# Performance work log

Hardware: AMD Instinct MI355X
Metric: run time of the kernel (lower is better)

Reference implementation:

```python
import jax, jax.numpy as jnp
import numpy as np

EPS = 1e-5
BANDLIMIT = 0.5
STEP_SCALE = 1.0


def _ln(x, g, b):
    mu = jnp.mean(x, axis=-1, keepdims=True)
    var = jnp.mean(jnp.square(x - mu), axis=-1, keepdims=True)
    return (x - mu) * jax.lax.rsqrt(var + EPS) * g + b


def _s5(u, Lambda_re, Lambda_im, B_re, B_im, C_re, C_im, D, log_step):
    # u: [N, T, C]; diagonal S5 SSM with ZOH discretization and parallel scan.
    Lam = Lambda_re + 1j * Lambda_im                      # [P] complex
    Bm = B_re + 1j * B_im                                  # [P, C]
    Cm = C_re + 1j * C_im                                  # [C, P]
    step = STEP_SCALE * jnp.exp(log_step)                  # [P]
    Lam_bar = jnp.exp(Lam * step)                          # [P]
    B_bar = ((Lam_bar - 1.0) / Lam)[:, None] * Bm          # [P, C]
    # bandlimit mask on output projection (freqs use un-scaled step)
    freqs = jnp.exp(log_step) * jnp.abs(Lambda_im) / (2.0 * jnp.pi)
    Cm = Cm * jnp.where(freqs < BANDLIMIT * 0.5, 1.0, 0.0)[None, :]
    Bu = jnp.einsum('ntc,pc->ntp', u.astype(B_bar.dtype), B_bar)  # [N,T,P] complex
    A = jnp.broadcast_to(Lam_bar, Bu.shape)

    def op(e1, e2):
        a1, b1 = e1
        a2, b2 = e2
        return a2 * a1, a2 * b1 + b2

    _, xs = jax.lax.associative_scan(op, (A, Bu), axis=1)   # x_t = Lam_bar*x_{t-1} + B_bar u_t (x_0 = 0)
    y = jnp.einsum('ntp,cp->ntc', xs, Cm).real + u * D
    return y


def setup_inputs() -> dict:
    key = jax.random.key(0)
    ks = jax.random.split(key, 16)
    B, T, H, W = 2, 15, 192, 192
    C, P = 16, 16
    sC = 1.0 / np.sqrt(C)
    sP = 1.0 / np.sqrt(P)
    inp = {}
    inp['x'] = jax.random.normal(ks[0], (B, T, H, W), dtype=jnp.float32)
    # input_proj: Linear(1, C)
    inp['w_in'] = jax.random.normal(ks[1], (C,), dtype=jnp.float32)
    inp['b_in'] = jnp.zeros((C,), dtype=jnp.float32)
    # S5Block attn_norm
    inp['attn_gamma'] = jnp.ones((C,), dtype=jnp.float32)
    inp['attn_beta'] = jnp.zeros((C,), dtype=jnp.float32)
    # S5 SSM parameters (stable: Re(Lambda) < 0)
    inp['Lambda_re'] = -jax.random.uniform(ks[2], (P,), jnp.float32, 0.1, 1.0)
    inp['Lambda_im'] = jnp.pi * jnp.arange(P, dtype=jnp.float32)
    inp['B_re'] = sC * jax.random.normal(ks[3], (P, C), dtype=jnp.float32)
    inp['B_im'] = sC * jax.random.normal(ks[4], (P, C), dtype=jnp.float32)
    inp['C_re'] = sP * jax.random.normal(ks[5], (C, P), dtype=jnp.float32)
    inp['C_im'] = sP * jax.random.normal(ks[6], (C, P), dtype=jnp.float32)
    inp['D'] = jax.random.normal(ks[7], (C,), dtype=jnp.float32)
    inp['log_step'] = jax.random.uniform(ks[8], (P,), jnp.float32, np.log(1e-3), np.log(0.1))
    # S5Block FFN (GEGLU, ff_mult=1.0, no bias)
    inp['ff_gamma'] = jnp.ones((C,), dtype=jnp.float32)
    inp['ff_beta'] = jnp.zeros((C,), dtype=jnp.float32)
    inp['W_enc'] = sC * jax.random.normal(ks[9], (2 * C, C), dtype=jnp.float32)
    inp['W_dec'] = sC * jax.random.normal(ks[10], (C, C), dtype=jnp.float32)
    # output_proj: LayerNorm(C) + Linear(C, C)
    inp['out_gamma'] = jnp.ones((C,), dtype=jnp.float32)
    inp['out_beta'] = jnp.zeros((C,), dtype=jnp.float32)
    inp['W_out'] = sC * jax.random.normal(ks[11], (C, C), dtype=jnp.float32)
    inp['b_out'] = jnp.zeros((C,), dtype=jnp.float32)
    return inp


def reference(x, w_in, b_in, attn_gamma, attn_beta, Lambda_re, Lambda_im,
              B_re, B_im, C_re, C_im, D, log_step,
              ff_gamma, ff_beta, W_enc, W_dec,
              out_gamma, out_beta, W_out, b_out):
    b, t, h, w = x.shape
    C = w_in.shape[0]
    # (b t h w) -> (b h w) t 1 -> Linear(1, C)
    u = jnp.transpose(x, (0, 2, 3, 1)).reshape(b * h * w, t)          # [N, T]
    u = u[:, :, None] * w_in + b_in                                     # [N, T, C]
    # --- S5Block ---
    fx = _ln(u, attn_gamma, attn_beta)
    s5_out = _s5(fx, Lambda_re, Lambda_im, B_re, B_im, C_re, C_im, D, log_step)
    z = jax.nn.gelu(s5_out, approximate=False) + fx
    fx2 = _ln(z, ff_gamma, ff_beta)
    enc = fx2 @ W_enc.T                                                 # [N, T, 2C]
    a, g = enc[..., :C], enc[..., C:]
    z2 = (a * jax.nn.gelu(g, approximate=False)) @ W_dec.T + fx2
    # aggregation = 'last'
    agg = z2[:, -1, :]                                                  # [N, C]
    # output_proj
    out = _ln(agg, out_gamma, out_beta) @ W_out.T + b_out               # [N, C]
    y = jnp.transpose(out.reshape(b, h, w, C), (0, 3, 1, 2))            # [B, C, H, W]
    return y
```

## Files before the change

### kernel.cpp

```cpp
#include <hip/hip_runtime.h>
#include <math.h>

#define HW_TOT 36864
#define T_LEN  15
#define NSEQ   73728


__device__ __forceinline__ float gelu_exact(float x){
  float ax = fabsf(x) * 0.7071067811865476f;
  float t  = 1.0f / (1.0f + 0.3275911f * ax);
  float poly = t*(0.254829592f + t*(-0.284496736f + t*(1.421413741f +
               t*(-1.453152027f + t*1.061405429f))));
  float er = 1.0f - poly * __expf(-ax*ax);
  er = copysignf(er, x);
  return 0.5f * x * (1.0f + er);
}

__global__ void __launch_bounds__(64) ssm_setup(
    const float* __restrict__ w_in, const float* __restrict__ b_in,
    const float* __restrict__ ag,   const float* __restrict__ ab,
    const float* __restrict__ Lre,  const float* __restrict__ Lim,
    const float* __restrict__ Bre,  const float* __restrict__ Bim,
    const float* __restrict__ Cre,  const float* __restrict__ Cim,
    const float* __restrict__ Dv,   const float* __restrict__ ls,
    const float* __restrict__ ffg,  const float* __restrict__ ffb,
    const float* __restrict__ Wenc, const float* __restrict__ Wdec,
    const float* __restrict__ og,   const float* __restrict__ ob,
    const float* __restrict__ Wout, const float* __restrict__ bout,
    float* __restrict__ ws)
{
  const int tid = threadIdx.x;

  float mw = 0.f, mb = 0.f;
  for (int c = 0; c < 16; ++c){ mw += w_in[c]; mb += b_in[c]; }
  mw *= 0.0625f; mb *= 0.0625f;
  float Saa = 0.f, Sad = 0.f, Sdd = 0.f;
  for (int c = 0; c < 16; ++c){
    float a = w_in[c]-mw, d = b_in[c]-mb;
    Saa += a*a; Sad += a*d; Sdd += d*d;
  }
  Saa *= 0.0625f; Sad *= 0.0625f; Sdd *= 0.0625f;
  if (tid == 0){ ws[128]=Saa; ws[129]=2.f*Sad; ws[130]=Sdd; ws[131]=0.f; }

  if (tid < 16){
    int c = tid;
    float a = w_in[c]-mw, d = b_in[c]-mb, g = ag[c];
    ws[132+c] = a*g;
    ws[148+c] = d*g;
    ws[164+c] = ab[c];
    ws[180+c] = Dv[c];
  }

  if (tid < 16){
    int p = tid;
    float step = expf(ls[p]);
    float lr = Lre[p], li = Lim[p];
    float er = expf(lr*step);
    float th = li*step;
    float Lbr = er*cosf(th), Lbi = er*sinf(th);
    ws[96+p] = Lbr; ws[112+p] = Lbi;
    float inv = 1.f/(lr*lr + li*li);
    float gr = Lbr - 1.f, gi = Lbi;
    float fr = (gr*lr + gi*li)*inv;
    float fi = (gi*lr - gr*li)*inv;
    float P1r=0,P1i=0,P2r=0,P2i=0,P3r=0,P3i=0;
    for (int c = 0; c < 16; ++c){
      float br = Bre[p*16+c], bi = Bim[p*16+c];
      float Bbr = fr*br - fi*bi, Bbi = fr*bi + fi*br;
      float a = w_in[c]-mw, d = b_in[c]-mb, g = ag[c];
      float f1 = a*g, f2 = d*g, f3 = ab[c];
      P1r += f1*Bbr; P1i += f1*Bbi;
      P2r += f2*Bbr; P2i += f2*Bbi;
      P3r += f3*Bbr; P3i += f3*Bbi;
    }
    ws[ 0+p]=P1r; ws[16+p]=P1i; ws[32+p]=P2r;
    ws[48+p]=P2i; ws[64+p]=P3r; ws[80+p]=P3i;
  }

  for (int k = tid; k < 256; k += 64){
    int p = k & 15;
    float step = expf(ls[p]);
    float freq = step * fabsf(Lim[p]) * 0.15915494309189535f;
    float m = (freq < 0.25f) ? 1.f : 0.f;
    ws[196+k] = Cre[k]*m;
    ws[452+k] = Cim[k]*m;
  }
  for (int k = tid; k < 512; k += 64) ws[ 708+k] = Wenc[k];
  for (int k = tid; k < 256; k += 64) ws[1220+k] = Wdec[k];
  for (int k = tid; k < 256; k += 64) ws[1540+k] = Wout[k];
  if (tid < 16){
    ws[1476+tid] = ffg[tid];
    ws[1492+tid] = ffb[tid];
    ws[1508+tid] = og[tid];
    ws[1524+tid] = ob[tid];
    ws[1796+tid] = bout[tid];
  }
}

__global__ void __launch_bounds__(64) ssm_main(
    const float* __restrict__ x, const float* __restrict__ ws,
    float* __restrict__ out)
{
  const int n   = blockIdx.x * 64 + threadIdx.x;
  const int b   = (n >= HW_TOT) ? 1 : 0;
  const int rem = n - b * HW_TOT;

  const float* xp = x + (size_t)b * (T_LEN * HW_TOT) + rem;
  float xv[T_LEN];
#pragma unroll
  for (int t = 0; t < T_LEN; ++t) xv[t] = xp[(size_t)t * HW_TOT];

  const float Saa = ws[128], Sad2 = ws[129], Sdd = ws[130];
  float P1r[16],P1i[16],P2r[16],P2i[16],P3r[16],P3i[16],Lr[16],Li[16];
#pragma unroll
  for (int p = 0; p < 16; ++p){
    P1r[p]=ws[p];    P1i[p]=ws[16+p];
    P2r[p]=ws[32+p]; P2i[p]=ws[48+p];
    P3r[p]=ws[64+p]; P3i[p]=ws[80+p];
    Lr[p] =ws[96+p]; Li[p] =ws[112+p];
  }

  float sre[16], sim_[16];
#pragma unroll
  for (int p = 0; p < 16; ++p){ sre[p]=0.f; sim_[p]=0.f; }

  float rstdL = 0.f, s1L = 0.f;
#pragma unroll
  for (int t = 0; t < T_LEN; ++t){
    const float xvt  = xv[t];
    const float var  = fmaf(xvt, fmaf(xvt, Saa, Sad2), Sdd);
    const float rstd = rsqrtf(var + 1e-5f);
    const float s1   = rstd * xvt;
#pragma unroll
    for (int p = 0; p < 16; ++p){
      const float br = fmaf(s1, P1r[p], fmaf(rstd, P2r[p], P3r[p]));
      const float bi = fmaf(s1, P1i[p], fmaf(rstd, P2i[p], P3i[p]));
      const float nr = fmaf(Lr[p], sre[p], fmaf(-Li[p], sim_[p], br));
      const float ni = fmaf(Lr[p], sim_[p], fmaf( Li[p], sre[p], bi));
      sre[p] = nr; sim_[p] = ni;
    }
    rstdL = rstd; s1L = s1;
  }

  float fx[16];
#pragma unroll
  for (int c = 0; c < 16; ++c)
    fx[c] = fmaf(s1L, ws[132+c], fmaf(rstdL, ws[148+c], ws[164+c]));

  float z[16];
#pragma unroll
  for (int c = 0; c < 16; ++c){
    float acc = fx[c] * ws[180+c];
#pragma unroll
    for (int p = 0; p < 16; ++p){
      acc = fmaf(sre[p],   ws[196 + c*16 + p], acc);
      acc = fmaf(-sim_[p], ws[452 + c*16 + p], acc);
    }
    z[c] = gelu_exact(acc) + fx[c];
  }

  float mu = 0.f;
#pragma unroll
  for (int c = 0; c < 16; ++c) mu += z[c];
  mu *= 0.0625f;
  float vr = 0.f;
#pragma unroll
  for (int c = 0; c < 16; ++c){ float d = z[c]-mu; vr = fmaf(d,d,vr); }
  vr *= 0.0625f;
  float rs = rsqrtf(vr + 1e-5f);
  float fx2[16];
#pragma unroll
  for (int c = 0; c < 16; ++c)
    fx2[c] = fmaf((z[c]-mu)*rs, ws[1476+c], ws[1492+c]);

  float hg[16];
#pragma unroll
  for (int c = 0; c < 16; ++c){
    float a = 0.f, g = 0.f;
#pragma unroll
    for (int k = 0; k < 16; ++k){
      a = fmaf(fx2[k], ws[708 + c*16 + k], a);
      g = fmaf(fx2[k], ws[708 + (16+c)*16 + k], g);
    }
    hg[c] = a * gelu_exact(g);
  }

  float z2[16];
#pragma unroll
  for (int c = 0; c < 16; ++c){
    float acc = fx2[c];
#pragma unroll
    for (int k = 0; k < 16; ++k) acc = fmaf(hg[k], ws[1220 + c*16 + k], acc);
    z2[c] = acc;
  }

  float mu3 = 0.f;
#pragma unroll
  for (int c = 0; c < 16; ++c) mu3 += z2[c];
  mu3 *= 0.0625f;
  float v3 = 0.f;
#pragma unroll
  for (int c = 0; c < 16; ++c){ float d = z2[c]-mu3; v3 = fmaf(d,d,v3); }
  v3 *= 0.0625f;
  float rs3 = rsqrtf(v3 + 1e-5f);
  float q[16];
#pragma unroll
  for (int c = 0; c < 16; ++c)
    q[c] = fmaf((z2[c]-mu3)*rs3, ws[1508+c], ws[1524+c]);

  float* op = out + (size_t)b * (16*HW_TOT) + rem;
#pragma unroll
  for (int c = 0; c < 16; ++c){
    float acc = ws[1796+c];
#pragma unroll
    for (int k = 0; k < 16; ++k) acc = fmaf(q[k], ws[1540 + c*16 + k], acc);
    op[(size_t)c * HW_TOT] = acc;
  }
}

extern "C" void kernel_launch(void* const* d_in, const int* in_sizes, int n_in,
                              void* d_out, int out_size, void* d_ws, size_t ws_size,
                              hipStream_t stream)
{
  const float* x    = (const float*)d_in[0];
  const float* w_in = (const float*)d_in[1];
  const float* b_in = (const float*)d_in[2];
  const float* ag   = (const float*)d_in[3];
  const float* ab   = (const float*)d_in[4];
  const float* Lre  = (const float*)d_in[5];
  const float* Lim  = (const float*)d_in[6];
  const float* Bre  = (const float*)d_in[7];
  const float* Bim  = (const float*)d_in[8];
  const float* Cre  = (const float*)d_in[9];
  const float* Cim  = (const float*)d_in[10];
  const float* Dv   = (const float*)d_in[11];
  const float* ls   = (const float*)d_in[12];
  const float* ffg  = (const float*)d_in[13];
  const float* ffb  = (const float*)d_in[14];
  const float* Wenc = (const float*)d_in[15];
  const float* Wdec = (const float*)d_in[16];
  const float* og   = (const float*)d_in[17];
  const float* ob   = (const float*)d_in[18];
  const float* Wout = (const float*)d_in[19];
  const float* bout = (const float*)d_in[20];
  float* ws  = (float*)d_ws;
  float* out = (float*)d_out;

  ssm_setup<<<1, 64, 0, stream>>>(w_in, b_in, ag, ab, Lre, Lim, Bre, Bim,
                                  Cre, Cim, Dv, ls, ffg, ffb, Wenc, Wdec,
                                  og, ob, Wout, bout, ws);
  ssm_main<<<NSEQ/64, 64, 0, stream>>>(x, ws, out);
}
```

Before: 135.1 us.

## Factor SSM scan into two input-driven recurrences and stage params in LDS

The per-step SSM input is split algebraically into a term scaled by s1, a term scaled by rstd, and a constant term. The constant term's scan contribution is precomputed in the setup kernel as a geometric sum. The main kernel then runs two scalar-driven complex recurrences and projects them through P1/P2 only once at the end, which drops the per-step complex B projections. All workspace parameters are also staged into shared memory per block instead of being read from global memory. This adds a block-wide copy and a barrier, and holds four complex accumulator arrays in registers.

```diff
diff --git a/kernel.cpp b/kernel.cpp
--- a/kernel.cpp
+++ b/kernel.cpp
@@ -4,6 +4,7 @@
 #define HW_TOT 36864
 #define T_LEN  15
 #define NSEQ   73728
+#define WS_N   1812
 
 
 __device__ __forceinline__ float gelu_exact(float x){
@@ -58,7 +59,7 @@
     float er = expf(lr*step);
     float th = li*step;
     float Lbr = er*cosf(th), Lbi = er*sinf(th);
-    ws[96+p] = Lbr; ws[112+p] = Lbi;
+    ws[0+p] = Lbr; ws[16+p] = Lbi;
     float inv = 1.f/(lr*lr + li*li);
     float gr = Lbr - 1.f, gi = Lbi;
     float fr = (gr*lr + gi*li)*inv;
@@ -73,8 +74,17 @@
       P2r += f2*Bbr; P2i += f2*Bbi;
       P3r += f3*Bbr; P3i += f3*Bbi;
     }
-    ws[ 0+p]=P1r; ws[16+p]=P1i; ws[32+p]=P2r;
-    ws[48+p]=P2i; ws[64+p]=P3r; ws[80+p]=P3i;
+    ws[32+p]=P1r; ws[48+p]=P1i;
+    ws[64+p]=P2r; ws[80+p]=P2i;
+    float kr=1.f, ki=0.f, cr_=1.f, ci_=0.f;
+    for (int j = 1; j < T_LEN; ++j){
+      float nr = cr_*Lbr - ci_*Lbi;
+      float ni = cr_*Lbi + ci_*Lbr;
+      cr_ = nr; ci_ = ni;
+      kr += cr_; ki += ci_;
+    }
+    ws[ 96+p] = P3r*kr - P3i*ki;
+    ws[112+p] = P3r*ki + P3i*kr;
   }
 
   for (int k = tid; k < 256; k += 64){
@@ -87,12 +97,12 @@
   }
   for (int k = tid; k < 512; k += 64) ws[ 708+k] = Wenc[k];
   for (int k = tid; k < 256; k += 64) ws[1220+k] = Wdec[k];
-  for (int k = tid; k < 256; k += 64) ws[1540+k] = Wout[k];
+  for (int k = tid; k < 256; k += 64) ws[1476+k] = Wout[k];
   if (tid < 16){
-    ws[1476+tid] = ffg[tid];
-    ws[1492+tid] = ffb[tid];
-    ws[1508+tid] = og[tid];
-    ws[1524+tid] = ob[tid];
+    ws[1732+tid] = ffg[tid];
+    ws[1748+tid] = ffb[tid];
+    ws[1764+tid] = og[tid];
+    ws[1780+tid] = ob[tid];
     ws[1796+tid] = bout[tid];
   }
 }
@@ -101,6 +111,9 @@
     const float* __restrict__ x, const float* __restrict__ ws,
     float* __restrict__ out)
 {
+  __shared__ float sm[WS_N];
+  for (int k = threadIdx.x; k < WS_N; k += 64) sm[k] = ws[k];
+
   const int n   = blockIdx.x * 64 + threadIdx.x;
   const int b   = (n >= HW_TOT) ? 1 : 0;
   const int rem = n - b * HW_TOT;
@@ -110,19 +123,16 @@
 #pragma unroll
   for (int t = 0; t < T_LEN; ++t) xv[t] = xp[(size_t)t * HW_TOT];
 
-  const float Saa = ws[128], Sad2 = ws[129], Sdd = ws[130];
-  float P1r[16],P1i[16],P2r[16],P2i[16],P3r[16],P3i[16],Lr[16],Li[16];
-#pragma unroll
-  for (int p = 0; p < 16; ++p){
-    P1r[p]=ws[p];    P1i[p]=ws[16+p];
-    P2r[p]=ws[32+p]; P2i[p]=ws[48+p];
-    P3r[p]=ws[64+p]; P3i[p]=ws[80+p];
-    Lr[p] =ws[96+p]; Li[p] =ws[112+p];
-  }
-
-  float sre[16], sim_[16];
-#pragma unroll
-  for (int p = 0; p < 16; ++p){ sre[p]=0.f; sim_[p]=0.f; }
+  __syncthreads();
+
+  float Lr[16], Li[16];
+#pragma unroll
+  for (int p = 0; p < 16; ++p){ Lr[p] = sm[p]; Li[p] = sm[16+p]; }
+  const float Saa = sm[128], Sad2 = sm[129], Sdd = sm[130];
+
+  float A1r[16], A1i[16], A2r[16], A2i[16];
+#pragma unroll
+  for (int p = 0; p < 16; ++p){ A1r[p]=0.f; A1i[p]=0.f; A2r[p]=0.f; A2i[p]=0.f; }
 
   float rstdL = 0.f, s1L = 0.f;
 #pragma unroll
@@ -133,28 +143,42 @@
     const float s1   = rstd * xvt;
 #pragma unroll
     for (int p = 0; p < 16; ++p){
-      const float br = fmaf(s1, P1r[p], fmaf(rstd, P2r[p], P3r[p]));
-      const float bi = fmaf(s1, P1i[p], fmaf(rstd, P2i[p], P3i[p]));
-      const float nr = fmaf(Lr[p], sre[p], fmaf(-Li[p], sim_[p], br));
-      const float ni = fmaf(Lr[p], sim_[p], fmaf( Li[p], sre[p], bi));
-      sre[p] = nr; sim_[p] = ni;
+      float n1r = fmaf(Lr[p], A1r[p], fmaf(-Li[p], A1i[p], s1));
+      float n1i = fmaf(Lr[p], A1i[p], Li[p]*A1r[p]);
+      A1r[p] = n1r; A1i[p] = n1i;
+      float n2r = fmaf(Lr[p], A2r[p], fmaf(-Li[p], A2i[p], rstd));
+      float n2i = fmaf(Lr[p], A2i[p], Li[p]*A2r[p]);
+      A2r[p] = n2r; A2i[p] = n2i;
     }
     rstdL = rstd; s1L = s1;
   }
 
+  float sre[16], sim_[16];
+#pragma unroll
+  for (int p = 0; p < 16; ++p){
+    float p1r = sm[32+p], p1i = sm[48+p];
+    float p2r = sm[64+p], p2i = sm[80+p];
+    float r = sm[96+p], im = sm[112+p];
+    r  = fmaf(p1r, A1r[p], fmaf(-p1i, A1i[p], r));
+    r  = fmaf(p2r, A2r[p], fmaf(-p2i, A2i[p], r));
+    im = fmaf(p1r, A1i[p], fmaf( p1i, A1r[p], im));
+    im = fmaf(p2r, A2i[p], fmaf( p2i, A2r[p], im));
+    sre[p] = r; sim_[p] = im;
+  }
+
   float fx[16];
 #pragma unroll
   for (int c = 0; c < 16; ++c)
-    fx[c] = fmaf(s1L, ws[132+c], fmaf(rstdL, ws[148+c], ws[164+c]));
+    fx[c] = fmaf(s1L, sm[132+c], fmaf(rstdL, sm[148+c], sm[164+c]));
 
   float z[16];
 #pragma unroll
   for (int c = 0; c < 16; ++c){
-    float acc = fx[c] * ws[180+c];
+    float acc = fx[c] * sm[180+c];
 #pragma unroll
     for (int p = 0; p < 16; ++p){
-      acc = fmaf(sre[p],   ws[196 + c*16 + p], acc);
-      acc = fmaf(-sim_[p], ws[452 + c*16 + p], acc);
+      acc = fmaf(sre[p],   sm[196 + c*16 + p], acc);
+      acc = fmaf(-sim_[p], sm[452 + c*16 + p], acc);
     }
     z[c] = gelu_exact(acc) + fx[c];
   }
@@ -171,7 +195,7 @@
   float fx2[16];
 #pragma unroll
   for (int c = 0; c < 16; ++c)
-    fx2[c] = fmaf((z[c]-mu)*rs, ws[1476+c], ws[1492+c]);
+    fx2[c] = fmaf((z[c]-mu)*rs, sm[1732+c], sm[1748+c]);
 
   float hg[16];
 #pragma unroll
@@ -179,8 +203,8 @@
     float a = 0.f, g = 0.f;
 #pragma unroll
     for (int k = 0; k < 16; ++k){
-      a = fmaf(fx2[k], ws[708 + c*16 + k], a);
-      g = fmaf(fx2[k], ws[708 + (16+c)*16 + k], g);
+      a = fmaf(fx2[k], sm[708 + c*16 + k], a);
+      g = fmaf(fx2[k], sm[708 + (16+c)*16 + k], g);
     }
     hg[c] = a * gelu_exact(g);
   }
@@ -190,7 +214,7 @@
   for (int c = 0; c < 16; ++c){
     float acc = fx2[c];
 #pragma unroll
-    for (int k = 0; k < 16; ++k) acc = fmaf(hg[k], ws[1220 + c*16 + k], acc);
+    for (int k = 0; k < 16; ++k) acc = fmaf(hg[k], sm[1220 + c*16 + k], acc);
     z2[c] = acc;
   }
 
@@ -203,17 +227,17 @@
   for (int c = 0; c < 16; ++c){ float d = z2[c]-mu3; v3 = fmaf(d,d,v3); }
   v3 *= 0.0625f;
   float rs3 = rsqrtf(v3 + 1e-5f);
-  float q[16];
+  float qv[16];
 #pragma unroll
   for (int c = 0; c < 16; ++c)
-    q[c] = fmaf((z2[c]-mu3)*rs3, ws[1508+c], ws[1524+c]);
+    qv[c] = fmaf((z2[c]-mu3)*rs3, sm[1764+c], sm[1780+c]);
 
   float* op = out + (size_t)b * (16*HW_TOT) + rem;
 #pragma unroll
   for (int c = 0; c < 16; ++c){
-    float acc = ws[1796+c];
-#pragma unroll
-    for (int k = 0; k < 16; ++k) acc = fmaf(q[k], ws[1540 + c*16 + k], acc);
+    float acc = sm[1796+c];
+#pragma unroll
+    for (int k = 0; k < 16; ++k) acc = fmaf(qv[k], sm[1476 + c*16 + k], acc);
     op[(size_t)c * HW_TOT] = acc;
   }
 }
```

New measurement: 122.4 us. 1.1x faster.

## Collapse SSM scan into precomputed per-timestep kernels and process two sequences per thread

Applied to the files above, without the earlier changes.

The setup kernel now precomputes, for each output channel and timestep, the combined effect of the input projection, Lambda powers and the masked C projection. The main kernel then computes the last-step SSM output as a linear combination of per-timestep terms, which replaces the 16-state complex recurrence and the C projection. The main kernel also stages the weight table in shared memory and handles two sequences per thread so each weight read is reused. This cuts per-thread arithmetic, but the grid shrinks to 576 blocks of 64 threads and register pressure rises.

```diff
diff --git a/kernel.cpp b/kernel.cpp
--- a/kernel.cpp
+++ b/kernel.cpp
@@ -4,7 +4,23 @@
 #define HW_TOT 36864
 #define T_LEN  15
 #define NSEQ   73728
-
+#define NBLK   576
+
+#define OFF_F1    4
+#define OFF_F2    20
+#define OFF_F3    36
+#define OFF_D     52
+#define OFF_G3    68
+#define OFF_G12   84
+#define OFF_WENC  596
+#define OFF_WDEC  1108
+#define OFF_WOUT  1364
+#define OFF_FFG   1620
+#define OFF_FFB   1636
+#define OFF_OG    1652
+#define OFF_OB    1668
+#define OFF_BOUT  1684
+#define SM_N      1700
 
 __device__ __forceinline__ float gelu_exact(float x){
   float ax = fabsf(x) * 0.7071067811865476f;
@@ -29,6 +45,8 @@
     const float* __restrict__ Wout, const float* __restrict__ bout,
     float* __restrict__ ws)
 {
+  __shared__ float U1r[240], U1i[240], U2r[240], U2i[240];
+  __shared__ float Cr[256], Ci[256], Qr[16], Qi[16];
   const int tid = threadIdx.x;
 
   float mw = 0.f, mb = 0.f;
@@ -40,15 +58,20 @@
     Saa += a*a; Sad += a*d; Sdd += d*d;
   }
   Saa *= 0.0625f; Sad *= 0.0625f; Sdd *= 0.0625f;
-  if (tid == 0){ ws[128]=Saa; ws[129]=2.f*Sad; ws[130]=Sdd; ws[131]=0.f; }
+  if (tid == 0){ ws[0]=Saa; ws[1]=2.f*Sad; ws[2]=Sdd; ws[3]=0.f; }
 
   if (tid < 16){
     int c = tid;
     float a = w_in[c]-mw, d = b_in[c]-mb, g = ag[c];
-    ws[132+c] = a*g;
-    ws[148+c] = d*g;
-    ws[164+c] = ab[c];
-    ws[180+c] = Dv[c];
+    ws[OFF_F1+c] = a*g;
+    ws[OFF_F2+c] = d*g;
+    ws[OFF_F3+c] = ab[c];
+    ws[OFF_D +c] = Dv[c];
+    ws[OFF_FFG+c] = ffg[c];
+    ws[OFF_FFB+c] = ffb[c];
+    ws[OFF_OG +c] = og[c];
+    ws[OFF_OB +c] = ob[c];
+    ws[OFF_BOUT+c] = bout[c];
   }
 
   if (tid < 16){
@@ -58,7 +81,6 @@
     float er = expf(lr*step);
     float th = li*step;
     float Lbr = er*cosf(th), Lbi = er*sinf(th);
-    ws[96+p] = Lbr; ws[112+p] = Lbi;
     float inv = 1.f/(lr*lr + li*li);
     float gr = Lbr - 1.f, gi = Lbi;
     float fr = (gr*lr + gi*li)*inv;
@@ -73,8 +95,23 @@
       P2r += f2*Bbr; P2i += f2*Bbi;
       P3r += f3*Bbr; P3i += f3*Bbi;
     }
-    ws[ 0+p]=P1r; ws[16+p]=P1i; ws[32+p]=P2r;
-    ws[48+p]=P2i; ws[64+p]=P3r; ws[80+p]=P3i;
+    float c1r=P1r, c1i=P1i, c2r=P2r, c2i=P2i;
+    U1r[p*15+0]=c1r; U1i[p*15+0]=c1i;
+    U2r[p*15+0]=c2r; U2i[p*15+0]=c2i;
+    float kr=1.f, ki=0.f, pr=1.f, pi=0.f;
+    for (int j = 1; j < T_LEN; ++j){
+      float t1r = c1r*Lbr - c1i*Lbi, t1i = c1r*Lbi + c1i*Lbr;
+      c1r=t1r; c1i=t1i;
+      U1r[p*15+j]=c1r; U1i[p*15+j]=c1i;
+      float t2r = c2r*Lbr - c2i*Lbi, t2i = c2r*Lbi + c2i*Lbr;
+      c2r=t2r; c2i=t2i;
+      U2r[p*15+j]=c2r; U2i[p*15+j]=c2i;
+      float tpr = pr*Lbr - pi*Lbi, tpi = pr*Lbi + pi*Lbr;
+      pr=tpr; pi=tpi;
+      kr += pr; ki += pi;
+    }
+    Qr[p] = P3r*kr - P3i*ki;
+    Qi[p] = P3r*ki + P3i*kr;
   }
 
   for (int k = tid; k < 256; k += 64){
@@ -82,18 +119,32 @@
     float step = expf(ls[p]);
     float freq = step * fabsf(Lim[p]) * 0.15915494309189535f;
     float m = (freq < 0.25f) ? 1.f : 0.f;
-    ws[196+k] = Cre[k]*m;
-    ws[452+k] = Cim[k]*m;
-  }
-  for (int k = tid; k < 512; k += 64) ws[ 708+k] = Wenc[k];
-  for (int k = tid; k < 256; k += 64) ws[1220+k] = Wdec[k];
-  for (int k = tid; k < 256; k += 64) ws[1540+k] = Wout[k];
+    Cr[k] = Cre[k]*m;
+    Ci[k] = Cim[k]*m;
+  }
+  for (int k = tid; k < 512; k += 64) ws[OFF_WENC+k] = Wenc[k];
+  for (int k = tid; k < 256; k += 64) ws[OFF_WDEC+k] = Wdec[k];
+  for (int k = tid; k < 256; k += 64) ws[OFF_WOUT+k] = Wout[k];
+
+  __syncthreads();
+
+  for (int idx = tid; idx < 240; idx += 64){
+    int c = idx / 15, t = idx - 15*c, j = 14 - t;
+    float g1 = 0.f, g2 = 0.f;
+    for (int p = 0; p < 16; ++p){
+      float cr = Cr[c*16+p], ci = Ci[c*16+p];
+      g1 = fmaf(cr, U1r[p*15+j], fmaf(-ci, U1i[p*15+j], g1));
+      g2 = fmaf(cr, U2r[p*15+j], fmaf(-ci, U2i[p*15+j], g2));
+    }
+    ws[OFF_G12 + c*32 + 2*t    ] = g1;
+    ws[OFF_G12 + c*32 + 2*t + 1] = g2;
+  }
   if (tid < 16){
-    ws[1476+tid] = ffg[tid];
-    ws[1492+tid] = ffb[tid];
-    ws[1508+tid] = og[tid];
-    ws[1524+tid] = ob[tid];
-    ws[1796+tid] = bout[tid];
+    int c = tid;
+    float g3 = 0.f;
+    for (int p = 0; p < 16; ++p)
+      g3 = fmaf(Cr[c*16+p], Qr[p], fmaf(-Ci[c*16+p], Qi[p], g3));
+    ws[OFF_G3+c] = g3;
   }
 }
 
@@ -101,120 +152,143 @@
     const float* __restrict__ x, const float* __restrict__ ws,
     float* __restrict__ out)
 {
-  const int n   = blockIdx.x * 64 + threadIdx.x;
-  const int b   = (n >= HW_TOT) ? 1 : 0;
-  const int rem = n - b * HW_TOT;
-
-  const float* xp = x + (size_t)b * (T_LEN * HW_TOT) + rem;
-  float xv[T_LEN];
-#pragma unroll
-  for (int t = 0; t < T_LEN; ++t) xv[t] = xp[(size_t)t * HW_TOT];
-
-  const float Saa = ws[128], Sad2 = ws[129], Sdd = ws[130];
-  float P1r[16],P1i[16],P2r[16],P2i[16],P3r[16],P3i[16],Lr[16],Li[16];
-#pragma unroll
-  for (int p = 0; p < 16; ++p){
-    P1r[p]=ws[p];    P1i[p]=ws[16+p];
-    P2r[p]=ws[32+p]; P2i[p]=ws[48+p];
-    P3r[p]=ws[64+p]; P3i[p]=ws[80+p];
-    Lr[p] =ws[96+p]; Li[p] =ws[112+p];
-  }
-
-  float sre[16], sim_[16];
-#pragma unroll
-  for (int p = 0; p < 16; ++p){ sre[p]=0.f; sim_[p]=0.f; }
-
-  float rstdL = 0.f, s1L = 0.f;
+  __shared__ float sm[SM_N];
+  const int tid = threadIdx.x;
+
+  const int n0 = blockIdx.x * 128 + tid;
+  const int n1 = n0 + 64;
+  const int b0 = (n0 >= HW_TOT) ? 1 : 0;
+  const int b1 = (n1 >= HW_TOT) ? 1 : 0;
+  const int r0 = n0 - b0 * HW_TOT;
+  const int r1 = n1 - b1 * HW_TOT;
+
+  const float* xp0 = x + (size_t)b0 * (T_LEN * HW_TOT) + r0;
+  const float* xp1 = x + (size_t)b1 * (T_LEN * HW_TOT) + r1;
+  float xv[2][T_LEN];
 #pragma unroll
   for (int t = 0; t < T_LEN; ++t){
-    const float xvt  = xv[t];
-    const float var  = fmaf(xvt, fmaf(xvt, Saa, Sad2), Sdd);
-    const float rstd = rsqrtf(var + 1e-5f);
-    const float s1   = rstd * xvt;
-#pragma unroll
-    for (int p = 0; p < 16; ++p){
-      const float br = fmaf(s1, P1r[p], fmaf(rstd, P2r[p], P3r[p]));
-      const float bi = fmaf(s1, P1i[p], fmaf(rstd, P2i[p], P3i[p]));
-      const float nr = fmaf(Lr[p], sre[p], fmaf(-Li[p], sim_[p], br));
-      const float ni = fmaf(Lr[p], sim_[p], fmaf( Li[p], sre[p], bi));
-      sre[p] = nr; sim_[p] = ni;
-    }
-    rstdL = rstd; s1L = s1;
-  }
-
-  float fx[16];
-#pragma unroll
-  for (int c = 0; c < 16; ++c)
-    fx[c] = fmaf(s1L, ws[132+c], fmaf(rstdL, ws[148+c], ws[164+c]));
-
-  float z[16];
-#pragma unroll
-  for (int c = 0; c < 16; ++c){
-    float acc = fx[c] * ws[180+c];
-#pragma unroll
-    for (int p = 0; p < 16; ++p){
-      acc = fmaf(sre[p],   ws[196 + c*16 + p], acc);
-      acc = fmaf(-sim_[p], ws[452 + c*16 + p], acc);
-    }
-    z[c] = gelu_exact(acc) + fx[c];
-  }
-
-  float mu = 0.f;
-#pragma unroll
-  for (int c = 0; c < 16; ++c) mu += z[c];
-  mu *= 0.0625f;
-  float vr = 0.f;
-#pragma unroll
-  for (int c = 0; c < 16; ++c){ float d = z[c]-mu; vr = fmaf(d,d,vr); }
-  vr *= 0.0625f;
-  float rs = rsqrtf(vr + 1e-5f);
-  float fx2[16];
-#pragma unroll
-  for (int c = 0; c < 16; ++c)
-    fx2[c] = fmaf((z[c]-mu)*rs, ws[1476+c], ws[1492+c]);
-
-  float hg[16];
-#pragma unroll
-  for (int c = 0; c < 16; ++c){
-    float a = 0.f, g = 0.f;
+    xv[0][t] = xp0[(size_t)t * HW_TOT];
+    xv[1][t] = xp1[(size_t)t * HW_TOT];
+  }
+
+  for (int k = tid; k < SM_N; k += 64) sm[k] = ws[k];
+  __syncthreads();
+
+  const float Saa = sm[0], Sad2 = sm[1], Sdd = sm[2];
+  float s1v[2][T_LEN], rsv[2][T_LEN];
+#pragma unroll
+  for (int s = 0; s < 2; ++s)
+#pragma unroll
+    for (int t = 0; t < T_LEN; ++t){
+      float xt   = xv[s][t];
+      float var  = fmaf(xt, fmaf(xt, Saa, Sad2), Sdd);
+      float rstd = rsqrtf(var + 1e-5f);
+      rsv[s][t] = rstd;
+      s1v[s][t] = rstd * xt;
+    }
+
+  float z[2][16];
+#pragma unroll
+  for (int c = 0; c < 16; ++c){
+    float a0 = sm[OFF_G3+c], a1 = a0;
+#pragma unroll
+    for (int t = 0; t < T_LEN; ++t){
+      float g1 = sm[OFF_G12 + c*32 + 2*t];
+      float g2 = sm[OFF_G12 + c*32 + 2*t + 1];
+      a0 = fmaf(s1v[0][t], g1, fmaf(rsv[0][t], g2, a0));
+      a1 = fmaf(s1v[1][t], g1, fmaf(rsv[1][t], g2, a1));
+    }
+    z[0][c] = a0; z[1][c] = a1;
+  }
+
+  float fx[2][16];
+#pragma unroll
+  for (int s = 0; s < 2; ++s){
+    const float s1L = s1v[s][T_LEN-1], rsL = rsv[s][T_LEN-1];
+#pragma unroll
+    for (int c = 0; c < 16; ++c){
+      float f = fmaf(s1L, sm[OFF_F1+c], fmaf(rsL, sm[OFF_F2+c], sm[OFF_F3+c]));
+      fx[s][c] = f;
+      float y = fmaf(f, sm[OFF_D+c], z[s][c]);
+      z[s][c] = gelu_exact(y) + f;
+    }
+  }
+
+  float fx2[2][16];
+#pragma unroll
+  for (int s = 0; s < 2; ++s){
+    float mu = 0.f;
+#pragma unroll
+    for (int c = 0; c < 16; ++c) mu += z[s][c];
+    mu *= 0.0625f;
+    float vr = 0.f;
+#pragma unroll
+    for (int c = 0; c < 16; ++c){ float d = z[s][c]-mu; vr = fmaf(d,d,vr); }
+    vr *= 0.0625f;
+    float rs = rsqrtf(vr + 1e-5f);
+#pragma unroll
+    for (int c = 0; c < 16; ++c)
+      fx2[s][c] = fmaf((z[s][c]-mu)*rs, sm[OFF_FFG+c], sm[OFF_FFB+c]);
+  }
+
+  float hg[2][16];
+#pragma unroll
+  for (int c = 0; c < 16; ++c){
+    float a0=0.f, g0=0.f, a1=0.f, g1=0.f;
 #pragma unroll
     for (int k = 0; k < 16; ++k){
-      a = fmaf(fx2[k], ws[708 + c*16 + k], a);
-      g = fmaf(fx2[k], ws[708 + (16+c)*16 + k], g);
-    }
-    hg[c] = a * gelu_exact(g);
-  }
-
-  float z2[16];
-#pragma unroll
-  for (int c = 0; c < 16; ++c){
-    float acc = fx2[c];
-#pragma unroll
-    for (int k = 0; k < 16; ++k) acc = fmaf(hg[k], ws[1220 + c*16 + k], acc);
-    z2[c] = acc;
-  }
-
-  float mu3 = 0.f;
-#pragma unroll
-  for (int c = 0; c < 16; ++c) mu3 += z2[c];
-  mu3 *= 0.0625f;
-  float v3 = 0.f;
-#pragma unroll
-  for (int c = 0; c < 16; ++c){ float d = z2[c]-mu3; v3 = fmaf(d,d,v3); }
-  v3 *= 0.0625f;
-  float rs3 = rsqrtf(v3 + 1e-5f);
-  float q[16];
-#pragma unroll
-  for (int c = 0; c < 16; ++c)
-    q[c] = fmaf((z2[c]-mu3)*rs3, ws[1508+c], ws[1524+c]);
-
-  float* op = out + (size_t)b * (16*HW_TOT) + rem;
-#pragma unroll
-  for (int c = 0; c < 16; ++c){
-    float acc = ws[1796+c];
-#pragma unroll
-    for (int k = 0; k < 16; ++k) acc = fmaf(q[k], ws[1540 + c*16 + k], acc);
-    op[(size_t)c * HW_TOT] = acc;
+      float wa = sm[OFF_WENC + c*16 + k];
+      float wg = sm[OFF_WENC + (16+c)*16 + k];
+      a0 = fmaf(fx2[0][k], wa, a0); g0 = fmaf(fx2[0][k], wg, g0);
+      a1 = fmaf(fx2[1][k], wa, a1); g1 = fmaf(fx2[1][k], wg, g1);
+    }
+    hg[0][c] = a0 * gelu_exact(g0);
+    hg[1][c] = a1 * gelu_exact(g1);
+  }
+
+  float z2[2][16];
+#pragma unroll
+  for (int c = 0; c < 16; ++c){
+    float acc0 = fx2[0][c], acc1 = fx2[1][c];
+#pragma unroll
+    for (int k = 0; k < 16; ++k){
+      float wd = sm[OFF_WDEC + c*16 + k];
+      acc0 = fmaf(hg[0][k], wd, acc0);
+      acc1 = fmaf(hg[1][k], wd, acc1);
+    }
+    z2[0][c] = acc0; z2[1][c] = acc1;
+  }
+
+  float qv[2][16];
+#pragma unroll
+  for (int s = 0; s < 2; ++s){
+    float mu = 0.f;
+#pragma unroll
+    for (int c = 0; c < 16; ++c) mu += z2[s][c];
+    mu *= 0.0625f;
+    float vr = 0.f;
+#pragma unroll
+    for (int c = 0; c < 16; ++c){ float d = z2[s][c]-mu; vr = fmaf(d,d,vr); }
+    vr *= 0.0625f;
+    float rs = rsqrtf(vr + 1e-5f);
+#pragma unroll
+    for (int c = 0; c < 16; ++c)
+      qv[s][c] = fmaf((z2[s][c]-mu)*rs, sm[OFF_OG+c], sm[OFF_OB+c]);
+  }
+
+  float* op0 = out + (size_t)b0 * (16*HW_TOT) + r0;
+  float* op1 = out + (size_t)b1 * (16*HW_TOT) + r1;
+#pragma unroll
+  for (int c = 0; c < 16; ++c){
+    float acc0 = sm[OFF_BOUT+c], acc1 = acc0;
+#pragma unroll
+    for (int k = 0; k < 16; ++k){
+      float wo = sm[OFF_WOUT + c*16 + k];
+      acc0 = fmaf(qv[0][k], wo, acc0);
+      acc1 = fmaf(qv[1][k], wo, acc1);
+    }
+    op0[(size_t)c * HW_TOT] = acc0;
+    op1[(size_t)c * HW_TOT] = acc1;
   }
 }
 
@@ -249,5 +323,5 @@
   ssm_setup<<<1, 64, 0, stream>>>(w_in, b_in, ag, ab, Lre, Lim, Bre, Bim,
                                   Cre, Cim, Dv, ls, ffg, ffb, Wenc, Wdec,
                                   og, ob, Wout, bout, ws);
-  ssm_main<<<NSEQ/64, 64, 0, stream>>>(x, ws, out);
+  ssm_main<<<NBLK, 64, 0, stream>>>(x, ws, out);
 }
```

Measured after the change: 118.4 us. 12.4% less time.
